# Performance work log

Measured on AMD Instinct MI355X. Metric: run time of the kernel, lower is better.

## Reference

```python
import jax, jax.numpy as jnp
import numpy as np

SEQ, IN_DIM, HID, CLS, BATCH = 512, 256, 2048, 1024, 256

def _xavier(key, shape):
    fan_in, fan_out = shape
    a = float(np.sqrt(6.0 / (fan_in + fan_out)))
    return jax.random.uniform(key, shape, jnp.float32, -a, a)

def setup_inputs() -> dict:
    key = jax.random.key(0)
    k1, k2, k3, k4 = jax.random.split(key, 4)
    return {
        "x": jax.random.normal(k1, (BATCH, SEQ, IN_DIM), jnp.float32),
        "Whx": _xavier(k2, (IN_DIM, HID)),
        "Whh": _xavier(k3, (HID, HID)),
        "Wph": _xavier(k4, (HID, CLS)),
        "Bh": jnp.zeros((HID,), jnp.float32),
        "Bp": jnp.zeros((CLS,), jnp.float32),
    }

def reference(x, Whx, Whh, Wph, Bh, Bp):
    # Precompute input projections for all steps in one big GEMM: [B,S,H]
    xp = jnp.einsum('bsi,ih->bsh', x, Whx) + Bh
    h0 = jnp.zeros((x.shape[0], Whh.shape[0]), x.dtype)

    def step(h, xp_t):
        h = jnp.tanh(xp_t + h @ Whh)
        return h, None

    h_final, _ = jax.lax.scan(step, h0, jnp.swapaxes(xp, 0, 1))  # scan over seq
    return h_final @ Wph + Bp  # logits from last timestep only
```

## Files before the change

### kernel.cpp

```cpp
#include <hip/hip_runtime.h>
#include <hip/hip_bf16.h>

typedef __attribute__((ext_vector_type(8))) short short8;
typedef __attribute__((ext_vector_type(4))) float f32x4;
typedef __attribute__((ext_vector_type(16))) float f32x16;
typedef __attribute__((ext_vector_type(4))) int i32x4;
typedef __attribute__((ext_vector_type(16))) int i32x16;
typedef unsigned long long u64;

#define MFMA16(A, B, C) __builtin_amdgcn_mfma_f32_16x16x32_bf16((A), (B), (C), 0, 0, 0)
#define MFMA32(A, B, C) __builtin_amdgcn_mfma_f32_32x32x16_bf16((A), (B), (C), 0, 0, 0)
#define MFMAI8(A, B, C) __builtin_amdgcn_mfma_i32_32x32x32_i8((A), (B), (C), 0, 0, 0)

static constexpr int kS = 512;
static constexpr int kI = 256;
static constexpr int kH = 2048;
static constexpr int kC = 1024;
static constexpr int kBt = 256;

static constexpr float kA   = 0.03828f;
static constexpr float kSW  = 127.0f / kA;
static constexpr float kINV = kA / (127.0f * 127.0f);

static constexpr int ZONE_OFF = 131072;

__device__ __forceinline__ int swz(int row, int kbyte) {
  return row * 4096 + (kbyte ^ ((row & 7) << 4));
}
__device__ __forceinline__ int swz8(int row, int kbyte) {
  return row * 2048 + (kbyte ^ ((row & 7) << 4));
}
__device__ __forceinline__ f32x4* zq(char* smem, int ci2, int quad, int slot, int lane) {
  return (f32x4*)(smem + ZONE_OFF + ((((ci2 * 4 + quad) * 3 + slot) * 64 + lane) << 4));
}
__device__ __forceinline__ f32x4* zslot2(char* smem, int row, int quad) {
  return (f32x4*)(smem + ZONE_OFF + row * 128 + (((quad ^ row) & 7) << 4));
}

__device__ __forceinline__ unsigned short f2bf(float f) {
  unsigned u = __float_as_uint(f);
  u += 0x7fffu + ((u >> 16) & 1u);
  return (unsigned short)(u >> 16);
}

__device__ __forceinline__ float fast_tanh(float v) {
  float a = __builtin_fabsf(v);
  float e = __expf(-2.0f * a);
  float r = (1.0f - e) / (1.0f + e);
  return __builtin_copysignf(r, v);
}

__device__ __forceinline__ signed char qw(float w) {
  int q = __float2int_rn(w * kSW);
  q = q > 127 ? 127 : (q < -127 ? -127 : q);
  return (signed char)q;
}

__device__ __forceinline__ u64 ld_h8(const u64* p) {
  return __hip_atomic_load(p, __ATOMIC_RELAXED, __HIP_MEMORY_SCOPE_AGENT);
}
__device__ __forceinline__ void st_h4(unsigned* p, unsigned v) {
  __hip_atomic_store(p, v, __ATOMIC_RELAXED, __HIP_MEMORY_SCOPE_AGENT);
}
__device__ __forceinline__ unsigned ld_flag(const unsigned* p) {
  return __hip_atomic_load(p, __ATOMIC_RELAXED, __HIP_MEMORY_SCOPE_AGENT);
}
__device__ __forceinline__ void st_flag(unsigned* p, unsigned v) {
  __hip_atomic_store(p, v, __ATOMIC_RELAXED, __HIP_MEMORY_SCOPE_AGENT);
}

__device__ __forceinline__ void gload_lds16(const void* g, void* l) {
  __builtin_amdgcn_global_load_lds(
      (const __attribute__((address_space(1))) void*)g,
      (__attribute__((address_space(3))) void*)l, 16, 0, 17);
}

__global__ __launch_bounds__(512, 2)
void rnn_fused(const float* __restrict__ x, const float* __restrict__ Whx,
               const float* __restrict__ Whh, const float* __restrict__ Wph,
               const float* __restrict__ Bh, const float* __restrict__ Bp,
               float* __restrict__ out,
               char* __restrict__ h0buf, char* __restrict__ h1buf,
               unsigned* __restrict__ flags) {
  extern __shared__ char smem[];
  const int tid = (int)threadIdx.x;
  const int lane = tid & 63;
  const int wv = tid >> 6;
  const int ci2 = wv & 1;
  const int kq = wv >> 1;
  const int wg = (int)blockIdx.x;
  const int rg = wg >> 5;
  const int cg = wg & 31;
  const int r0 = rg * 32;
  const int n0 = cg * 64;

  const int j32 = lane & 31;
  const int hi = lane >> 5;
  const int wcol2 = n0 + ci2 * 32 + j32;

  union ifrag { i32x4 v; signed char b[16]; };
  ifrag wa[16];
#pragma unroll
  for (int ks = 0; ks < 16; ++ks) {
    const int kbase = (ks < 8) ? (kq * 256 + ks * 32)
                               : (1024 + kq * 256 + (ks - 8) * 32);
    const float* wp = Whh + (size_t)(kbase + hi * 16) * kH + wcol2;
    ifrag f;
#pragma unroll
    for (int jj = 0; jj < 16; ++jj) f.b[jj] = qw(wp[(size_t)jj * kH]);
    wa[ks] = f;
  }
  short8 wx[4];
#pragma unroll
  for (int ks = 0; ks < 4; ++ks) {
    const float* wp = Whx + (size_t)(kq * 64 + ks * 16 + hi * 8) * kH + wcol2;
#pragma unroll
    for (int jj = 0; jj < 8; ++jj) wx[ks][jj] = (short)f2bf(wp[(size_t)jj * kH]);
  }

  const f32x4 bh = *(const f32x4*)(Bh + n0 + ci2 * 32 + 8 * kq + 4 * hi);

  const int laneoff = lane * 16;
  unsigned* gflags = flags + (rg << 5);
  const float* px_row = x + (size_t)(r0 + j32) * (kS * kI);

  for (int t = 0; t < kS; ++t) {
    const char* hc = (t & 1) ? h1buf : h0buf;
    char* hn       = (t & 1) ? h0buf : h1buf;
    f32x16 facc = {0.f,0.f,0.f,0.f,0.f,0.f,0.f,0.f,0.f,0.f,0.f,0.f,0.f,0.f,0.f,0.f};
    i32x16 iacc = {0,0,0,0,0,0,0,0,0,0,0,0,0,0,0,0};

#pragma unroll
    for (int ks = 0; ks < 4; ++ks) {
      const int k = kq * 64 + ks * 16 + hi * 8;
      f32x4 xa = *(const f32x4*)(px_row + (size_t)t * kI + k);
      f32x4 xb = *(const f32x4*)(px_row + (size_t)t * kI + k + 4);
      short8 bx;
#pragma unroll
      for (int jj = 0; jj < 4; ++jj) {
        bx[jj] = (short)f2bf(xa[jj]); bx[jj + 4] = (short)f2bf(xb[jj]);
      }
      facc = MFMA32(wx[ks], bx, facc);
    }

    if (t > 0 && wv == 0) {
      while (!__all((int)(ld_flag(&gflags[lane & 31]) >= (unsigned)t)))
        __builtin_amdgcn_s_sleep(2);
      asm volatile("" ::: "memory");
    }
    __syncthreads();

#pragma unroll
    for (int jj = 0; jj < 8; ++jj) {
      const int half = jj >> 2;
      const int row = 4 * wv + (jj & 3);
      const char* gp = hc + (size_t)(r0 + row) * 2048 + half * 1024 +
                       (laneoff ^ ((row & 7) << 4));
      gload_lds16(gp, smem + row * 2048 + half * 1024);
    }
    asm volatile("s_waitcnt vmcnt(4)" ::: "memory");
    __builtin_amdgcn_sched_barrier(0);
    __builtin_amdgcn_s_barrier();
    __builtin_amdgcn_sched_barrier(0);

#pragma unroll
    for (int ks = 0; ks < 8; ++ks) {
      const int kb = kq * 256 + ks * 32 + hi * 16;
      i32x4 hb = *(const i32x4*)(smem + swz8(j32, kb));
      iacc = MFMAI8(wa[ks].v, hb, iacc);
    }
    asm volatile("s_waitcnt vmcnt(0)" ::: "memory");
    __builtin_amdgcn_sched_barrier(0);
    __builtin_amdgcn_s_barrier();
    __builtin_amdgcn_sched_barrier(0);

#pragma unroll
    for (int ks = 8; ks < 16; ++ks) {
      const int kb = 1024 + kq * 256 + (ks - 8) * 32 + hi * 16;
      i32x4 hb = *(const i32x4*)(smem + swz8(j32, kb));
      iacc = MFMAI8(wa[ks].v, hb, iacc);
    }

    f32x16 cacc;
#pragma unroll
    for (int jj = 0; jj < 16; ++jj) cacc[jj] = facc[jj] + (float)iacc[jj] * kINV;

#pragma unroll
    for (int qp = 0; qp < 4; ++qp) {
      if (qp != kq) {
        f32x4 part = {cacc[4 * qp], cacc[4 * qp + 1], cacc[4 * qp + 2], cacc[4 * qp + 3]};
        *zq(smem, ci2, qp, kq - (kq > qp ? 1 : 0), lane) = part;
      }
    }
    __syncthreads();

    {
      f32x4 s0 = *zq(smem, ci2, kq, 0, lane);
      f32x4 s1 = *zq(smem, ci2, kq, 1, lane);
      f32x4 s2 = *zq(smem, ci2, kq, 2, lane);
      unsigned pk = 0;
#pragma unroll
      for (int jj = 0; jj < 4; ++jj) {
        float sum = cacc[4 * kq + jj] + s0[jj] + s1[jj] + s2[jj] + bh[jj];
        int q = __float2int_rn(fast_tanh(sum) * 127.0f);
        pk |= ((unsigned)q & 0xFFu) << (8 * jj);
      }
      const int col = n0 + ci2 * 32 + 8 * kq + 4 * hi;
      st_h4((unsigned*)(hn + (size_t)(r0 + j32) * 2048 + col), pk);
    }

    __syncthreads();
    if (tid == 0) st_flag(&gflags[cg], (unsigned)(t + 1));
  }

  if (wv == 0) {
    while (!__all((int)(ld_flag(&gflags[lane & 31]) >= (unsigned)kS)))
      __builtin_amdgcn_s_sleep(2);
    asm volatile("" ::: "memory");
  }
  __syncthreads();

  {
    const int c = tid & 31;
    const int kk = tid >> 5;
    for (int k = kk; k < kH; k += 16)
      *(unsigned short*)(smem + swz(c, k * 2)) = f2bf(Wph[(size_t)k * kC + cg * 32 + c]);
  }
  __syncthreads();

  const int brow = lane & 15;
  const int nq = lane >> 4;
  const int klo = nq * 8;
  const bool act = (wv < 4);
  const int ci16 = wv & 1;
  const int kh2 = (wv >> 1) & 1;
  f32x4 oacc0 = {0.f, 0.f, 0.f, 0.f};
  f32x4 oacc1 = {0.f, 0.f, 0.f, 0.f};
  if (act) {
    const char* phA = h0buf + (size_t)(r0 + brow) * 2048;
    const char* phB = h0buf + (size_t)(r0 + 16 + brow) * 2048;
#pragma unroll 8
    for (int kt = 0; kt < 32; ++kt) {
      const int gk = kh2 * 1024 + kt * 32 + klo;
      short8 a = *(const short8*)(smem + swz(ci16 * 16 + brow, gk * 2));
      union { u64 q; signed char b[8]; } ua, ub;
      ua.q = ld_h8((const u64*)(phA + gk));
      ub.q = ld_h8((const u64*)(phB + gk));
      short8 ha, hb;
#pragma unroll
      for (int jj = 0; jj < 8; ++jj) {
        ha[jj] = (short)f2bf((float)ua.b[jj] * (1.0f / 127.0f));
        hb[jj] = (short)f2bf((float)ub.b[jj] * (1.0f / 127.0f));
      }
      oacc0 = MFMA16(a, ha, oacc0);
      oacc1 = MFMA16(a, hb, oacc1);
    }
  }
  if (act && kh2 == 1) {
    *zslot2(smem, brow, ci16 * 4 + nq) = oacc0;
    *zslot2(smem, brow + 16, ci16 * 4 + nq) = oacc1;
  }
  __syncthreads();
  if (act && kh2 == 0) {
    f32x4 s0 = *zslot2(smem, brow, ci16 * 4 + nq);
    f32x4 s1 = *zslot2(smem, brow + 16, ci16 * 4 + nq);
    const int ocol = cg * 32 + ci16 * 16 + nq * 4;
    const f32x4 bp = *(const f32x4*)(Bp + ocol);
#pragma unroll
    for (int jj = 0; jj < 4; ++jj) {
      out[(size_t)(r0 + brow) * kC + ocol + jj] = oacc0[jj] + s0[jj] + bp[jj];
      out[(size_t)(r0 + 16 + brow) * kC + ocol + jj] = oacc1[jj] + s1[jj] + bp[jj];
    }
  }
}

extern "C" void kernel_launch(void* const* d_in, const int* in_sizes, int n_in,
                              void* d_out, int out_size, void* d_ws, size_t ws_size,
                              hipStream_t stream) {
  const float* x   = (const float*)d_in[0];
  const float* Whx = (const float*)d_in[1];
  const float* Whh = (const float*)d_in[2];
  const float* Wph = (const float*)d_in[3];
  const float* Bh  = (const float*)d_in[4];
  const float* Bp  = (const float*)d_in[5];
  float* out = (float*)d_out;

  char* ws = (char*)d_ws;
  char* h0        = ws;
  char* h1        = ws + (1 << 19);
  unsigned* flags = (unsigned*)(ws + (1 << 20));

  hipMemsetAsync(h0, 0, (size_t)kBt * kH, stream);
  hipMemsetAsync(flags, 0, 4096, stream);

  dim3 grid(256), block(512);
  size_t lds = 155648;
  hipLaunchKernelGGL(rnn_fused, grid, block, lds, stream,
                     x, Whx, Whh, Wph, Bh, Bp, out, h0, h1, flags);
}
```

Baseline: 2.498 ms.

## Retile recurrent step to 16x128 per block with full-K per wave

Changes the block tile from 32 rows x 64 hidden columns to 16 rows x 128 columns and gives each wave the full K range using 16x16x64 int8 MFMAs. This removes the cross-wave split-K reduction through LDS and one __syncthreads per timestep, and halves the number of blocks each block must wait on per step (16 flags instead of 32). In exchange each wave holds twice as many quantized weight fragments in registers, and the final projection now loops over two column panels.

```diff
diff --git a/kernel.cpp b/kernel.cpp
--- a/kernel.cpp
+++ b/kernel.cpp
@@ -3,14 +3,11 @@
 
 typedef __attribute__((ext_vector_type(8))) short short8;
 typedef __attribute__((ext_vector_type(4))) float f32x4;
-typedef __attribute__((ext_vector_type(16))) float f32x16;
 typedef __attribute__((ext_vector_type(4))) int i32x4;
-typedef __attribute__((ext_vector_type(16))) int i32x16;
 typedef unsigned long long u64;
 
 #define MFMA16(A, B, C) __builtin_amdgcn_mfma_f32_16x16x32_bf16((A), (B), (C), 0, 0, 0)
-#define MFMA32(A, B, C) __builtin_amdgcn_mfma_f32_32x32x16_bf16((A), (B), (C), 0, 0, 0)
-#define MFMAI8(A, B, C) __builtin_amdgcn_mfma_i32_32x32x32_i8((A), (B), (C), 0, 0, 0)
+#define MFMAI8(A, B, C) __builtin_amdgcn_mfma_i32_16x16x64_i8((A), (B), (C), 0, 0, 0)
 
 static constexpr int kS = 512;
 static constexpr int kI = 256;
@@ -30,11 +27,8 @@
 __device__ __forceinline__ int swz8(int row, int kbyte) {
   return row * 2048 + (kbyte ^ ((row & 7) << 4));
 }
-__device__ __forceinline__ f32x4* zq(char* smem, int ci2, int quad, int slot, int lane) {
-  return (f32x4*)(smem + ZONE_OFF + ((((ci2 * 4 + quad) * 3 + slot) * 64 + lane) << 4));
-}
-__device__ __forceinline__ f32x4* zslot2(char* smem, int row, int quad) {
-  return (f32x4*)(smem + ZONE_OFF + row * 128 + (((quad ^ row) & 7) << 4));
+__device__ __forceinline__ f32x4* zep(char* smem, int cb, int slot, int lane) {
+  return (f32x4*)(smem + ZONE_OFF + (((cb * 3 + slot) * 64 + lane) << 4));
 }
 
 __device__ __forceinline__ unsigned short f2bf(float f) {
@@ -86,53 +80,50 @@
   const int tid = (int)threadIdx.x;
   const int lane = tid & 63;
   const int wv = tid >> 6;
-  const int ci2 = wv & 1;
-  const int kq = wv >> 1;
   const int wg = (int)blockIdx.x;
-  const int rg = wg >> 5;
-  const int cg = wg & 31;
-  const int r0 = rg * 32;
-  const int n0 = cg * 64;
-
-  const int j32 = lane & 31;
-  const int hi = lane >> 5;
-  const int wcol2 = n0 + ci2 * 32 + j32;
+  const int rg = wg >> 4;
+  const int cg = wg & 15;
+  const int r0 = rg * 16;
+  const int n0 = cg * 128;
+
+  const int a16 = lane & 15;
+  const int kb16 = lane >> 4;
+  const int wcol = n0 + wv * 16 + a16;
 
   union ifrag { i32x4 v; signed char b[16]; };
-  ifrag wa[16];
-#pragma unroll
-  for (int ks = 0; ks < 16; ++ks) {
-    const int kbase = (ks < 8) ? (kq * 256 + ks * 32)
-                               : (1024 + kq * 256 + (ks - 8) * 32);
-    const float* wp = Whh + (size_t)(kbase + hi * 16) * kH + wcol2;
+  ifrag wa[32];
+#pragma unroll
+  for (int ks = 0; ks < 32; ++ks) {
+    const int kwin = (ks < 16) ? ks * 64 : 1024 + (ks - 16) * 64;
     ifrag f;
 #pragma unroll
-    for (int jj = 0; jj < 16; ++jj) f.b[jj] = qw(wp[(size_t)jj * kH]);
+    for (int jj = 0; jj < 16; ++jj)
+      f.b[jj] = qw(Whh[(size_t)(kwin + kb16 * 16 + jj) * kH + wcol]);
     wa[ks] = f;
   }
-  short8 wx[4];
-#pragma unroll
-  for (int ks = 0; ks < 4; ++ks) {
-    const float* wp = Whx + (size_t)(kq * 64 + ks * 16 + hi * 8) * kH + wcol2;
-#pragma unroll
-    for (int jj = 0; jj < 8; ++jj) wx[ks][jj] = (short)f2bf(wp[(size_t)jj * kH]);
-  }
-
-  const f32x4 bh = *(const f32x4*)(Bh + n0 + ci2 * 32 + 8 * kq + 4 * hi);
+  short8 wx[8];
+#pragma unroll
+  for (int ks = 0; ks < 8; ++ks) {
+#pragma unroll
+    for (int jj = 0; jj < 8; ++jj)
+      wx[ks][jj] = (short)f2bf(Whx[(size_t)(ks * 32 + kb16 * 8 + jj) * kH + wcol]);
+  }
+
+  const f32x4 bh = *(const f32x4*)(Bh + n0 + wv * 16 + kb16 * 4);
 
   const int laneoff = lane * 16;
-  unsigned* gflags = flags + (rg << 5);
-  const float* px_row = x + (size_t)(r0 + j32) * (kS * kI);
+  unsigned* gflags = flags + (rg << 4);
+  const float* px_row = x + (size_t)(r0 + a16) * (kS * kI);
 
   for (int t = 0; t < kS; ++t) {
     const char* hc = (t & 1) ? h1buf : h0buf;
     char* hn       = (t & 1) ? h0buf : h1buf;
-    f32x16 facc = {0.f,0.f,0.f,0.f,0.f,0.f,0.f,0.f,0.f,0.f,0.f,0.f,0.f,0.f,0.f,0.f};
-    i32x16 iacc = {0,0,0,0,0,0,0,0,0,0,0,0,0,0,0,0};
-
-#pragma unroll
-    for (int ks = 0; ks < 4; ++ks) {
-      const int k = kq * 64 + ks * 16 + hi * 8;
+    f32x4 facc = {0.f, 0.f, 0.f, 0.f};
+    i32x4 iacc = {0, 0, 0, 0};
+
+#pragma unroll
+    for (int ks = 0; ks < 8; ++ks) {
+      const int k = ks * 32 + kb16 * 8;
       f32x4 xa = *(const f32x4*)(px_row + (size_t)t * kI + k);
       f32x4 xb = *(const f32x4*)(px_row + (size_t)t * kI + k + 4);
       short8 bx;
@@ -140,33 +131,34 @@
       for (int jj = 0; jj < 4; ++jj) {
         bx[jj] = (short)f2bf(xa[jj]); bx[jj + 4] = (short)f2bf(xb[jj]);
       }
-      facc = MFMA32(wx[ks], bx, facc);
+      facc = MFMA16(wx[ks], bx, facc);
     }
 
     if (t > 0 && wv == 0) {
-      while (!__all((int)(ld_flag(&gflags[lane & 31]) >= (unsigned)t)))
+      while (!__all((int)(lane >= 16 ||
+                          ld_flag(&gflags[lane & 15]) >= (unsigned)t)))
         __builtin_amdgcn_s_sleep(2);
       asm volatile("" ::: "memory");
     }
     __syncthreads();
 
 #pragma unroll
-    for (int jj = 0; jj < 8; ++jj) {
-      const int half = jj >> 2;
-      const int row = 4 * wv + (jj & 3);
+    for (int jj = 0; jj < 4; ++jj) {
+      const int half = jj >> 1;
+      const int row = 2 * wv + (jj & 1);
       const char* gp = hc + (size_t)(r0 + row) * 2048 + half * 1024 +
                        (laneoff ^ ((row & 7) << 4));
       gload_lds16(gp, smem + row * 2048 + half * 1024);
     }
-    asm volatile("s_waitcnt vmcnt(4)" ::: "memory");
+    asm volatile("s_waitcnt vmcnt(2)" ::: "memory");
     __builtin_amdgcn_sched_barrier(0);
     __builtin_amdgcn_s_barrier();
     __builtin_amdgcn_sched_barrier(0);
 
 #pragma unroll
-    for (int ks = 0; ks < 8; ++ks) {
-      const int kb = kq * 256 + ks * 32 + hi * 16;
-      i32x4 hb = *(const i32x4*)(smem + swz8(j32, kb));
+    for (int ks = 0; ks < 16; ++ks) {
+      const int kb = ks * 64 + kb16 * 16;
+      i32x4 hb = *(const i32x4*)(smem + swz8(a16, kb));
       iacc = MFMAI8(wa[ks].v, hb, iacc);
     }
     asm volatile("s_waitcnt vmcnt(0)" ::: "memory");
@@ -175,38 +167,22 @@
     __builtin_amdgcn_sched_barrier(0);
 
 #pragma unroll
-    for (int ks = 8; ks < 16; ++ks) {
-      const int kb = 1024 + kq * 256 + (ks - 8) * 32 + hi * 16;
-      i32x4 hb = *(const i32x4*)(smem + swz8(j32, kb));
+    for (int ks = 16; ks < 32; ++ks) {
+      const int kb = 1024 + (ks - 16) * 64 + kb16 * 16;
+      i32x4 hb = *(const i32x4*)(smem + swz8(a16, kb));
       iacc = MFMAI8(wa[ks].v, hb, iacc);
     }
 
-    f32x16 cacc;
-#pragma unroll
-    for (int jj = 0; jj < 16; ++jj) cacc[jj] = facc[jj] + (float)iacc[jj] * kINV;
-
-#pragma unroll
-    for (int qp = 0; qp < 4; ++qp) {
-      if (qp != kq) {
-        f32x4 part = {cacc[4 * qp], cacc[4 * qp + 1], cacc[4 * qp + 2], cacc[4 * qp + 3]};
-        *zq(smem, ci2, qp, kq - (kq > qp ? 1 : 0), lane) = part;
-      }
-    }
-    __syncthreads();
-
     {
-      f32x4 s0 = *zq(smem, ci2, kq, 0, lane);
-      f32x4 s1 = *zq(smem, ci2, kq, 1, lane);
-      f32x4 s2 = *zq(smem, ci2, kq, 2, lane);
       unsigned pk = 0;
 #pragma unroll
       for (int jj = 0; jj < 4; ++jj) {
-        float sum = cacc[4 * kq + jj] + s0[jj] + s1[jj] + s2[jj] + bh[jj];
+        float sum = facc[jj] + (float)iacc[jj] * kINV + bh[jj];
         int q = __float2int_rn(fast_tanh(sum) * 127.0f);
         pk |= ((unsigned)q & 0xFFu) << (8 * jj);
       }
-      const int col = n0 + ci2 * 32 + 8 * kq + 4 * hi;
-      st_h4((unsigned*)(hn + (size_t)(r0 + j32) * 2048 + col), pk);
+      st_h4((unsigned*)(hn + (size_t)(r0 + a16) * 2048 + n0 + wv * 16 + kb16 * 4),
+            pk);
     }
 
     __syncthreads();
@@ -214,63 +190,54 @@
   }
 
   if (wv == 0) {
-    while (!__all((int)(ld_flag(&gflags[lane & 31]) >= (unsigned)kS)))
+    while (!__all((int)(lane >= 16 ||
+                        ld_flag(&gflags[lane & 15]) >= (unsigned)kS)))
       __builtin_amdgcn_s_sleep(2);
     asm volatile("" ::: "memory");
   }
   __syncthreads();
 
-  {
-    const int c = tid & 31;
-    const int kk = tid >> 5;
-    for (int k = kk; k < kH; k += 16)
-      *(unsigned short*)(smem + swz(c, k * 2)) = f2bf(Wph[(size_t)k * kC + cg * 32 + c]);
-  }
-  __syncthreads();
-
-  const int brow = lane & 15;
-  const int nq = lane >> 4;
-  const int klo = nq * 8;
-  const bool act = (wv < 4);
-  const int ci16 = wv & 1;
-  const int kh2 = (wv >> 1) & 1;
-  f32x4 oacc0 = {0.f, 0.f, 0.f, 0.f};
-  f32x4 oacc1 = {0.f, 0.f, 0.f, 0.f};
-  if (act) {
-    const char* phA = h0buf + (size_t)(r0 + brow) * 2048;
-    const char* phB = h0buf + (size_t)(r0 + 16 + brow) * 2048;
+  const int cb = wv & 1;
+  const int kqe = wv >> 1;
+#pragma unroll
+  for (int p = 0; p < 2; ++p) {
+    {
+      const int c = tid & 31;
+      const int kk = tid >> 5;
+      for (int k = kk; k < kH; k += 16)
+        *(unsigned short*)(smem + swz(c, k * 2)) =
+            f2bf(Wph[(size_t)k * kC + cg * 64 + p * 32 + c]);
+    }
+    __syncthreads();
+
+    f32x4 oacc = {0.f, 0.f, 0.f, 0.f};
+    const char* ph = h0buf + (size_t)(r0 + a16) * 2048;
 #pragma unroll 8
-    for (int kt = 0; kt < 32; ++kt) {
-      const int gk = kh2 * 1024 + kt * 32 + klo;
-      short8 a = *(const short8*)(smem + swz(ci16 * 16 + brow, gk * 2));
-      union { u64 q; signed char b[8]; } ua, ub;
-      ua.q = ld_h8((const u64*)(phA + gk));
-      ub.q = ld_h8((const u64*)(phB + gk));
-      short8 ha, hb;
-#pragma unroll
-      for (int jj = 0; jj < 8; ++jj) {
+    for (int kt = 0; kt < 16; ++kt) {
+      const int gk = kqe * 512 + kt * 32 + kb16 * 8;
+      short8 a = *(const short8*)(smem + swz(cb * 16 + a16, gk * 2));
+      union { u64 q; signed char b[8]; } ua;
+      ua.q = ld_h8((const u64*)(ph + gk));
+      short8 ha;
+#pragma unroll
+      for (int jj = 0; jj < 8; ++jj)
         ha[jj] = (short)f2bf((float)ua.b[jj] * (1.0f / 127.0f));
-        hb[jj] = (short)f2bf((float)ub.b[jj] * (1.0f / 127.0f));
-      }
-      oacc0 = MFMA16(a, ha, oacc0);
-      oacc1 = MFMA16(a, hb, oacc1);
-    }
-  }
-  if (act && kh2 == 1) {
-    *zslot2(smem, brow, ci16 * 4 + nq) = oacc0;
-    *zslot2(smem, brow + 16, ci16 * 4 + nq) = oacc1;
-  }
-  __syncthreads();
-  if (act && kh2 == 0) {
-    f32x4 s0 = *zslot2(smem, brow, ci16 * 4 + nq);
-    f32x4 s1 = *zslot2(smem, brow + 16, ci16 * 4 + nq);
-    const int ocol = cg * 32 + ci16 * 16 + nq * 4;
-    const f32x4 bp = *(const f32x4*)(Bp + ocol);
-#pragma unroll
-    for (int jj = 0; jj < 4; ++jj) {
-      out[(size_t)(r0 + brow) * kC + ocol + jj] = oacc0[jj] + s0[jj] + bp[jj];
-      out[(size_t)(r0 + 16 + brow) * kC + ocol + jj] = oacc1[jj] + s1[jj] + bp[jj];
-    }
+      oacc = MFMA16(a, ha, oacc);
+    }
+    if (kqe > 0) *zep(smem, cb, kqe - 1, lane) = oacc;
+    __syncthreads();
+    if (kqe == 0) {
+      f32x4 s0 = *zep(smem, cb, 0, lane);
+      f32x4 s1 = *zep(smem, cb, 1, lane);
+      f32x4 s2 = *zep(smem, cb, 2, lane);
+      const int ocol = cg * 64 + p * 32 + cb * 16 + kb16 * 4;
+      const int orow = r0 + a16;
+#pragma unroll
+      for (int jj = 0; jj < 4; ++jj)
+        out[(size_t)orow * kC + ocol + jj] =
+            oacc[jj] + s0[jj] + s1[jj] + s2[jj] + Bp[ocol + jj];
+    }
+    __syncthreads();
   }
 }
 
@@ -294,7 +261,7 @@
   hipMemsetAsync(flags, 0, 4096, stream);
 
   dim3 grid(256), block(512);
-  size_t lds = 155648;
+  size_t lds = 139264;
   hipLaunchKernelGGL(rnn_fused, grid, block, lds, stream,
                      x, Whx, Whh, Wph, Bh, Bp, out, h0, h1, flags);
 }
```

Result: slower. 3.376 ms (+35.2%).
